# Kernel optimization log

Hardware: AMD Instinct MI355X
Metric: run time of the kernel (lower is better)

The kernel has to match this reference:

```python
import jax, jax.numpy as jnp
import numpy as np

BS, INPUT_LEN, OUTPUT_LEN, H, OUT = 256, 512, 64, 1024, 64


def setup_inputs() -> dict:
    key = jax.random.key(0)
    ks = jax.random.split(key, 13)
    s = 1.0 / np.sqrt(H)
    si = 1.0 / np.sqrt(INPUT_LEN)
    return {
        "is_training": 0,
        "qf_encoded": jax.random.normal(ks[0], (BS, INPUT_LEN, H), jnp.float32),
        "op_encoded": jax.random.normal(ks[1], (BS, OUTPUT_LEN, H), jnp.float32),
        "vocab": jax.random.normal(ks[2], (64, H), jnp.float32),  # unused buffer, kept for fidelity
        "start_token": jax.random.normal(ks[3], (1, H), jnp.float32),
        "w_in": jax.random.uniform(ks[4], (INPUT_LEN,), jnp.float32, -si, si),  # in_proj weight [1, input_len]
        "b_in": jax.random.uniform(ks[5], (1,), jnp.float32, -si, si),
        "w_ih": jax.random.uniform(ks[6], (4 * H, H), jnp.float32, -s, s),
        "w_hh": jax.random.uniform(ks[7], (4 * H, H), jnp.float32, -s, s),
        "b_ih": jax.random.uniform(ks[8], (4 * H,), jnp.float32, -s, s),
        "b_hh": jax.random.uniform(ks[9], (4 * H,), jnp.float32, -s, s),
        "w_out": jax.random.uniform(ks[10], (OUT, H), jnp.float32, -s, s),
        "b_out": jax.random.uniform(ks[11], (OUT,), jnp.float32, -s, s),
    }


def reference(is_training, qf_encoded, op_encoded, vocab, start_token,
              w_in, b_in, w_ih, w_hh, b_ih, b_hh, w_out, b_out):
    # Inference path: dropout is identity, teacher forcing branch never taken
    # (is_training == 0). Attention over the single-step hidden state is
    # computed faithfully even though softmax over a length-1 axis yields 1.
    bs = qf_encoded.shape[0]
    # h0 = in_proj(qf_encoded.transpose(1,2)).squeeze(2): contract over input_len
    h0 = jnp.einsum("bih,i->bh", qf_encoded, w_in) + b_in  # [bs, H]
    c0 = jnp.zeros((bs, H), qf_encoded.dtype)
    x0 = jnp.broadcast_to(start_token, (bs, H))

    def step(carry, _):
        h, c, x = carry
        gates = x @ w_ih.T + b_ih + h @ w_hh.T + b_hh  # [bs, 4H]
        i_g, f_g, g_g, o_g = jnp.split(gates, 4, axis=1)
        c = jax.nn.sigmoid(f_g) * c + jax.nn.sigmoid(i_g) * jnp.tanh(g_g)
        h = jax.nn.sigmoid(o_g) * jnp.tanh(c)
        # attention(x[:,None], h[:,None], h[:,None]): scores [bs,1,1]
        scores = jnp.einsum("bh,bh->b", x, h)[:, None, None]
        w = jax.nn.softmax(scores, axis=2)  # all ones (length-1 softmax)
        x_new = w[:, 0] * h  # [bs,1]*[bs,H] -> [bs,H]
        return (h, c, x_new), h

    (_, _, _), hs = jax.lax.scan(step, (h0, c0, x0), None, length=OUTPUT_LEN)
    output = jnp.transpose(hs, (1, 0, 2))  # [bs, output_len, H]
    probs = output @ w_out.T + b_out  # [bs, output_len, output_size]
    return (probs, output)
```

## Files before the change

### kernel.cpp

```cpp
#include <hip/hip_runtime.h>

#define BS 256
#define IN_LEN 512
#define T_OUT 64
#define H 1024
#define G4 4096

typedef __attribute__((ext_vector_type(8))) short bf16x8;
typedef __attribute__((ext_vector_type(4))) float f32x4;

__device__ __forceinline__ unsigned short f2bf(float x) {
    union { float f; unsigned u; } v; v.f = x;
    unsigned r = v.u + 0x7fffu + ((v.u >> 16) & 1u);
    return (unsigned short)(r >> 16);
}
__device__ __forceinline__ float bf2f(unsigned short b) {
    union { unsigned u; float f; } v; v.u = ((unsigned)b) << 16;
    return v.f;
}
__device__ __forceinline__ float sigf(float x) { return 1.f / (1.f + __expf(-x)); }
__device__ __forceinline__ float tanhfast(float x) { return 1.f - 2.f / (__expf(2.f * x) + 1.f); }

__device__ __forceinline__ void gl_lds16(const void* g, void* l) {
    __builtin_amdgcn_global_load_lds((const __attribute__((address_space(1))) void*)g,
                                     (__attribute__((address_space(3))) void*)l, 16, 0, 0);
}

__global__ __launch_bounds__(256) void k_prep(const float4* __restrict__ w_ih4,
                                              const float4* __restrict__ w_hh4,
                                              const float4* __restrict__ w_out4,
                                              ushort4* __restrict__ Wch, ushort4* __restrict__ Wcl,
                                              ushort4* __restrict__ woh, ushort4* __restrict__ wol) {
    int row = blockIdx.x;
    int c4 = threadIdx.x;
    float4 a = w_ih4[row * 256 + c4];
    float4 b = w_hh4[row * 256 + c4];
    int p = ((row & 1023) << 2) | (row >> 10);
    float sx = a.x + b.x, sy = a.y + b.y, sz = a.z + b.z, sw = a.w + b.w;
    ushort4 hi, lo;
    hi.x = f2bf(sx); lo.x = f2bf(sx - bf2f(hi.x));
    hi.y = f2bf(sy); lo.y = f2bf(sy - bf2f(hi.y));
    hi.z = f2bf(sz); lo.z = f2bf(sz - bf2f(hi.z));
    hi.w = f2bf(sw); lo.w = f2bf(sw - bf2f(hi.w));
    Wch[p * 256 + c4] = hi;
    Wcl[p * 256 + c4] = lo;
    if (row < 64) {
        float4 w = w_out4[row * 256 + c4];
        ushort4 h2, l2;
        h2.x = f2bf(w.x); l2.x = f2bf(w.x - bf2f(h2.x));
        h2.y = f2bf(w.y); l2.y = f2bf(w.y - bf2f(h2.y));
        h2.z = f2bf(w.z); l2.z = f2bf(w.z - bf2f(h2.z));
        h2.w = f2bf(w.w); l2.w = f2bf(w.w - bf2f(h2.w));
        woh[row * 256 + c4] = h2;
        wol[row * 256 + c4] = l2;
    }
}

__global__ __launch_bounds__(256) void k_g0(const float4* __restrict__ st4,
                                            const float4* __restrict__ w_ih4,
                                            const float* __restrict__ b_ih,
                                            const float* __restrict__ b_hh,
                                            float* __restrict__ g0p, float* __restrict__ bcp) {
    int j = (blockIdx.x * 256 + threadIdx.x) >> 6;
    int lane = threadIdx.x & 63;
    float s = 0.f;
#pragma unroll
    for (int q = 0; q < 4; ++q) {
        int idx = q * 64 + lane;
        float4 w4 = w_ih4[(size_t)j * 256 + idx];
        float4 s4 = st4[idx];
        s += w4.x * s4.x + w4.y * s4.y + w4.z * s4.z + w4.w * s4.w;
    }
#pragma unroll
    for (int off = 32; off > 0; off >>= 1) s += __shfl_down(s, off, 64);
    if (lane == 0) {
        int p = ((j & 1023) << 2) | (j >> 10);
        float bb = b_ih[j] + b_hh[j];
        bcp[p] = bb;
        g0p[p] = s + bb;
    }
}

__global__ __launch_bounds__(256) void k_h0(const float4* __restrict__ qf4,
                                            const float* __restrict__ w_in,
                                            const float* __restrict__ b_in,
                                            ushort4* __restrict__ h_hi, ushort4* __restrict__ h_lo,
                                            float4* __restrict__ c4) {
    int idx = blockIdx.x * 256 + threadIdx.x;
    int b = idx >> 8;
    int hq = idx & 255;
    const float4* p = qf4 + (size_t)b * IN_LEN * 256 + hq;
    float4 s = make_float4(0.f, 0.f, 0.f, 0.f);
#pragma unroll 4
    for (int i = 0; i < IN_LEN; ++i) {
        float w = w_in[i];
        float4 q = p[(size_t)i * 256];
        s.x += q.x * w; s.y += q.y * w; s.z += q.z * w; s.w += q.w * w;
    }
    float bi = b_in[0];
    s.x += bi; s.y += bi; s.z += bi; s.w += bi;
    ushort4 hi, lo;
    hi.x = f2bf(s.x); lo.x = f2bf(s.x - bf2f(hi.x));
    hi.y = f2bf(s.y); lo.y = f2bf(s.y - bf2f(hi.y));
    hi.z = f2bf(s.z); lo.z = f2bf(s.z - bf2f(hi.z));
    hi.w = f2bf(s.w); lo.w = f2bf(s.w - bf2f(hi.w));
    h_hi[idx] = hi;
    h_lo[idx] = lo;
    c4[idx] = make_float4(0.f, 0.f, 0.f, 0.f);
}

__global__ __launch_bounds__(256) void k_step(const ushort* __restrict__ Bh,
                                              const ushort* __restrict__ Bl,
                                              const float* __restrict__ Bf,
                                              const float* __restrict__ bias,
                                              const ushort* __restrict__ Ah,
                                              const ushort* __restrict__ Al,
                                              float* __restrict__ c,
                                              ushort* __restrict__ Oh, ushort* __restrict__ Ol,
                                              float* __restrict__ out_h, int t, int useF32) {
    __shared__ __align__(16) ushort sAh[64 * 32], sAl[64 * 32], sBh[64 * 32], sBl[64 * 32];
    __shared__ __align__(16) float sC[64 * 68];

    const int tid = threadIdx.x;
    const int n0 = blockIdx.x * 64;
    const int m0 = blockIdx.y * 64;
    const int w = tid >> 6, l = tid & 63;
    const int wm = w & 1, wn = w >> 1;
    const int lm = l & 15, kg = l >> 4;

    const int srow = tid >> 2;
    const int scol = (tid & 3) * 8;
    const int ldsOff = (tid >> 6) * 512;

    const ushort* gAh = Ah + (m0 + srow) * H + scol;
    const ushort* gAl = Al + (m0 + srow) * H + scol;
    const int prow = n0 + srow;
    const ushort* gBh = Bh + prow * H + scol;
    const ushort* gBl = Bl + prow * H + scol;
    const float* gBf = Bf + ((prow & 3) * H + (prow >> 2)) * H + scol;

    f32x4 acc[2][2];
#pragma unroll
    for (int mi = 0; mi < 2; ++mi)
#pragma unroll
        for (int ni = 0; ni < 2; ++ni) acc[mi][ni] = (f32x4)(0.f);

#pragma unroll 1
    for (int ch = 0; ch < H / 32; ++ch) {
        const int k0 = ch * 32;
        __syncthreads();
        if (useF32) {
            float4 f0 = *(const float4*)(gBf + k0);
            float4 f1 = *(const float4*)(gBf + k0 + 4);
            ushort4 h0_, h1_, l0_, l1_;
            h0_.x = f2bf(f0.x); l0_.x = f2bf(f0.x - bf2f(h0_.x));
            h0_.y = f2bf(f0.y); l0_.y = f2bf(f0.y - bf2f(h0_.y));
            h0_.z = f2bf(f0.z); l0_.z = f2bf(f0.z - bf2f(h0_.z));
            h0_.w = f2bf(f0.w); l0_.w = f2bf(f0.w - bf2f(h0_.w));
            h1_.x = f2bf(f1.x); l1_.x = f2bf(f1.x - bf2f(h1_.x));
            h1_.y = f2bf(f1.y); l1_.y = f2bf(f1.y - bf2f(h1_.y));
            h1_.z = f2bf(f1.z); l1_.z = f2bf(f1.z - bf2f(h1_.z));
            h1_.w = f2bf(f1.w); l1_.w = f2bf(f1.w - bf2f(h1_.w));
            int si = srow * 32 + (tid & 3) * 8;
            *(ushort4*)&sBh[si] = h0_; *(ushort4*)&sBh[si + 4] = h1_;
            *(ushort4*)&sBl[si] = l0_; *(ushort4*)&sBl[si + 4] = l1_;
        } else {
            gl_lds16(gBh + k0, &sBh[ldsOff]);
            gl_lds16(gBl + k0, &sBl[ldsOff]);
        }
        gl_lds16(gAh + k0, &sAh[ldsOff]);
        gl_lds16(gAl + k0, &sAl[ldsOff]);
        __syncthreads();

        bf16x8 ah[2], al[2], bh[2], bl[2];
#pragma unroll
        for (int mi = 0; mi < 2; ++mi) {
            int base = (wm * 32 + mi * 16 + lm) * 32 + kg * 8;
            ah[mi] = *(const bf16x8*)&sAh[base];
            al[mi] = *(const bf16x8*)&sAl[base];
        }
#pragma unroll
        for (int ni = 0; ni < 2; ++ni) {
            int base = (wn * 32 + ni * 16 + lm) * 32 + kg * 8;
            bh[ni] = *(const bf16x8*)&sBh[base];
            bl[ni] = *(const bf16x8*)&sBl[base];
        }
#pragma unroll
        for (int mi = 0; mi < 2; ++mi)
#pragma unroll
            for (int ni = 0; ni < 2; ++ni) {
                acc[mi][ni] = __builtin_amdgcn_mfma_f32_16x16x32_bf16(ah[mi], bh[ni], acc[mi][ni], 0, 0, 0);
                acc[mi][ni] = __builtin_amdgcn_mfma_f32_16x16x32_bf16(ah[mi], bl[ni], acc[mi][ni], 0, 0, 0);
                acc[mi][ni] = __builtin_amdgcn_mfma_f32_16x16x32_bf16(al[mi], bh[ni], acc[mi][ni], 0, 0, 0);
            }
    }

#pragma unroll
    for (int mi = 0; mi < 2; ++mi)
#pragma unroll
        for (int ni = 0; ni < 2; ++ni) {
            int r0 = wm * 32 + mi * 16 + kg * 4;
            int c0_ = wn * 32 + ni * 16 + lm;
#pragma unroll
            for (int r = 0; r < 4; ++r) sC[(r0 + r) * 68 + c0_] = acc[mi][ni][r];
        }
    __syncthreads();

#pragma unroll
    for (int q = 0; q < 4; ++q) {
        int cid = tid + q * 256;
        int bl_ = cid >> 4, hl = cid & 15;
        float4 gv = *(const float4*)&sC[bl_ * 68 + hl * 4];
        float4 bv = *(const float4*)&bias[n0 + hl * 4];
        int b = m0 + bl_;
        int hh = (n0 >> 2) + hl;
        float cold = c[b * H + hh];
        float ig = gv.x + bv.x, fg = gv.y + bv.y, gg = gv.z + bv.z, og = gv.w + bv.w;
        float cn = sigf(fg) * cold + sigf(ig) * tanhfast(gg);
        float hn = sigf(og) * tanhfast(cn);
        c[b * H + hh] = cn;
        unsigned short hb = f2bf(hn);
        Oh[b * H + hh] = hb;
        Ol[b * H + hh] = f2bf(hn - bf2f(hb));
        out_h[(b * T_OUT + t) * H + hh] = hn;
    }
}

__global__ __launch_bounds__(256) void k_probs(const float* __restrict__ hs,
                                               const ushort* __restrict__ Bh,
                                               const ushort* __restrict__ Bl,
                                               const float* __restrict__ b_out,
                                               float* __restrict__ probs) {
    __shared__ __align__(16) ushort sAh[64 * 32], sAl[64 * 32], sBh[64 * 32], sBl[64 * 32];
    const int tid = threadIdx.x;
    const int r0 = blockIdx.x * 64;
    const int w = tid >> 6, l = tid & 63;
    const int wm = w & 1, wn = w >> 1;
    const int lm = l & 15, kg = l >> 4;
    const int srow = tid >> 2;
    const int scol = (tid & 3) * 8;
    const int ldsOff = (tid >> 6) * 512;

    const float* gA = hs + (size_t)(r0 + srow) * H + scol;
    const ushort* gBh = Bh + srow * H + scol;
    const ushort* gBl = Bl + srow * H + scol;

    f32x4 acc[2][2];
#pragma unroll
    for (int mi = 0; mi < 2; ++mi)
#pragma unroll
        for (int ni = 0; ni < 2; ++ni) acc[mi][ni] = (f32x4)(0.f);

#pragma unroll 1
    for (int ch = 0; ch < H / 32; ++ch) {
        const int k0 = ch * 32;
        __syncthreads();
        gl_lds16(gBh + k0, &sBh[ldsOff]);
        gl_lds16(gBl + k0, &sBl[ldsOff]);
        float4 f0 = *(const float4*)(gA + k0);
        float4 f1 = *(const float4*)(gA + k0 + 4);
        ushort4 h0_, h1_, l0_, l1_;
        h0_.x = f2bf(f0.x); l0_.x = f2bf(f0.x - bf2f(h0_.x));
        h0_.y = f2bf(f0.y); l0_.y = f2bf(f0.y - bf2f(h0_.y));
        h0_.z = f2bf(f0.z); l0_.z = f2bf(f0.z - bf2f(h0_.z));
        h0_.w = f2bf(f0.w); l0_.w = f2bf(f0.w - bf2f(h0_.w));
        h1_.x = f2bf(f1.x); l1_.x = f2bf(f1.x - bf2f(h1_.x));
        h1_.y = f2bf(f1.y); l1_.y = f2bf(f1.y - bf2f(h1_.y));
        h1_.z = f2bf(f1.z); l1_.z = f2bf(f1.z - bf2f(h1_.z));
        h1_.w = f2bf(f1.w); l1_.w = f2bf(f1.w - bf2f(h1_.w));
        int si = srow * 32 + (tid & 3) * 8;
        *(ushort4*)&sAh[si] = h0_; *(ushort4*)&sAh[si + 4] = h1_;
        *(ushort4*)&sAl[si] = l0_; *(ushort4*)&sAl[si + 4] = l1_;
        __syncthreads();

        bf16x8 ah[2], al[2], bh[2], bl[2];
#pragma unroll
        for (int mi = 0; mi < 2; ++mi) {
            int base = (wm * 32 + mi * 16 + lm) * 32 + kg * 8;
            ah[mi] = *(const bf16x8*)&sAh[base];
            al[mi] = *(const bf16x8*)&sAl[base];
        }
#pragma unroll
        for (int ni = 0; ni < 2; ++ni) {
            int base = (wn * 32 + ni * 16 + lm) * 32 + kg * 8;
            bh[ni] = *(const bf16x8*)&sBh[base];
            bl[ni] = *(const bf16x8*)&sBl[base];
        }
#pragma unroll
        for (int mi = 0; mi < 2; ++mi)
#pragma unroll
            for (int ni = 0; ni < 2; ++ni) {
                acc[mi][ni] = __builtin_amdgcn_mfma_f32_16x16x32_bf16(ah[mi], bh[ni], acc[mi][ni], 0, 0, 0);
                acc[mi][ni] = __builtin_amdgcn_mfma_f32_16x16x32_bf16(ah[mi], bl[ni], acc[mi][ni], 0, 0, 0);
                acc[mi][ni] = __builtin_amdgcn_mfma_f32_16x16x32_bf16(al[mi], bh[ni], acc[mi][ni], 0, 0, 0);
            }
    }

#pragma unroll
    for (int mi = 0; mi < 2; ++mi)
#pragma unroll
        for (int ni = 0; ni < 2; ++ni) {
            int col = wn * 32 + ni * 16 + lm;
            float bo = b_out[col];
            int rowb = r0 + wm * 32 + mi * 16 + kg * 4;
#pragma unroll
            for (int r = 0; r < 4; ++r)
                probs[(size_t)(rowb + r) * 64 + col] = acc[mi][ni][r] + bo;
        }
}

extern "C" void kernel_launch(void* const* d_in, const int* in_sizes, int n_in,
                              void* d_out, int out_size, void* d_ws, size_t ws_size,
                              hipStream_t stream) {
    const float* qf    = (const float*)d_in[1];
    const float* st    = (const float*)d_in[4];
    const float* w_in  = (const float*)d_in[5];
    const float* b_in  = (const float*)d_in[6];
    const float* w_ih  = (const float*)d_in[7];
    const float* w_hh  = (const float*)d_in[8];
    const float* b_ih  = (const float*)d_in[9];
    const float* b_hh  = (const float*)d_in[10];
    const float* w_out = (const float*)d_in[11];
    const float* b_out = (const float*)d_in[12];

    float* probs = (float*)d_out;
    float* out_h = probs + (size_t)BS * T_OUT * 64;

    char* ws = (char*)d_ws;
    ushort* Wch = (ushort*)ws; ws += (size_t)G4 * H * 2;
    ushort* Wcl = (ushort*)ws; ws += (size_t)G4 * H * 2;
    ushort* woh = (ushort*)ws; ws += (size_t)64 * H * 2;
    ushort* wol = (ushort*)ws; ws += (size_t)64 * H * 2;
    float*  bcp = (float*)ws;  ws += G4 * 4;
    float*  g0p = (float*)ws;  ws += G4 * 4;
    ushort* hAh = (ushort*)ws; ws += (size_t)BS * H * 2;
    ushort* hAl = (ushort*)ws; ws += (size_t)BS * H * 2;
    ushort* hBh = (ushort*)ws; ws += (size_t)BS * H * 2;
    ushort* hBl = (ushort*)ws; ws += (size_t)BS * H * 2;
    float*  cb  = (float*)ws;  ws += (size_t)BS * H * 4;

    k_prep<<<G4, 256, 0, stream>>>((const float4*)w_ih, (const float4*)w_hh, (const float4*)w_out,
                                   (ushort4*)Wch, (ushort4*)Wcl, (ushort4*)woh, (ushort4*)wol);
    k_g0<<<G4 / 4, 256, 0, stream>>>((const float4*)st, (const float4*)w_ih, b_ih, b_hh, g0p, bcp);
    k_h0<<<BS * H / 4 / 256, 256, 0, stream>>>((const float4*)qf, w_in, b_in,
                                               (ushort4*)hAh, (ushort4*)hAl, (float4*)cb);

    for (int t = 0; t < T_OUT; ++t) {
        const ushort* Ah = (t & 1) ? hBh : hAh;
        const ushort* Al = (t & 1) ? hBl : hAl;
        ushort* Oh = (t & 1) ? hAh : hBh;
        ushort* Ol = (t & 1) ? hAl : hBl;
        k_step<<<dim3(64, 4), 256, 0, stream>>>(Wch, Wcl, w_hh,
                                                (t == 0) ? g0p : bcp,
                                                Ah, Al, cb, Oh, Ol, out_h, t, (t == 0) ? 1 : 0);
    }
    k_probs<<<BS * T_OUT / 64, 256, 0, stream>>>(out_h, woh, wol, b_out, probs);
}
```

Baseline: 2.171 ms.

## Fuse LSTM steps and output projection into one persistent cooperative kernel

```diff
diff --git a/kernel.cpp b/kernel.cpp
--- a/kernel.cpp
+++ b/kernel.cpp
@@ -1,10 +1,15 @@
 #include <hip/hip_runtime.h>
+#include <hip/hip_cooperative_groups.h>
+
+namespace cg = cooperative_groups;
 
 #define BS 256
 #define IN_LEN 512
 #define T_OUT 64
 #define H 1024
 #define G4 4096
+#define BK 64
+#define NCH (H / BK)
 
 typedef __attribute__((ext_vector_type(8))) short bf16x8;
 typedef __attribute__((ext_vector_type(4))) float f32x4;
@@ -26,10 +31,14 @@
                                      (__attribute__((address_space(3))) void*)l, 16, 0, 0);
 }
 
+#define FRAG(base, row, ko) \
+    (*(const bf16x8*)((const char*)(base) + ((((row) * 128 + (ko)) ^ ((((row) & 7)) << 4)))))
+
 __global__ __launch_bounds__(256) void k_prep(const float4* __restrict__ w_ih4,
                                               const float4* __restrict__ w_hh4,
                                               const float4* __restrict__ w_out4,
                                               ushort4* __restrict__ Wch, ushort4* __restrict__ Wcl,
+                                              ushort4* __restrict__ Whh, ushort4* __restrict__ Whl,
                                               ushort4* __restrict__ woh, ushort4* __restrict__ wol) {
     int row = blockIdx.x;
     int c4 = threadIdx.x;
@@ -44,15 +53,22 @@
     hi.w = f2bf(sw); lo.w = f2bf(sw - bf2f(hi.w));
     Wch[p * 256 + c4] = hi;
     Wcl[p * 256 + c4] = lo;
+    ushort4 h2, l2;
+    h2.x = f2bf(b.x); l2.x = f2bf(b.x - bf2f(h2.x));
+    h2.y = f2bf(b.y); l2.y = f2bf(b.y - bf2f(h2.y));
+    h2.z = f2bf(b.z); l2.z = f2bf(b.z - bf2f(h2.z));
+    h2.w = f2bf(b.w); l2.w = f2bf(b.w - bf2f(h2.w));
+    Whh[p * 256 + c4] = h2;
+    Whl[p * 256 + c4] = l2;
     if (row < 64) {
         float4 w = w_out4[row * 256 + c4];
-        ushort4 h2, l2;
-        h2.x = f2bf(w.x); l2.x = f2bf(w.x - bf2f(h2.x));
-        h2.y = f2bf(w.y); l2.y = f2bf(w.y - bf2f(h2.y));
-        h2.z = f2bf(w.z); l2.z = f2bf(w.z - bf2f(h2.z));
-        h2.w = f2bf(w.w); l2.w = f2bf(w.w - bf2f(h2.w));
-        woh[row * 256 + c4] = h2;
-        wol[row * 256 + c4] = l2;
+        ushort4 h3, l3;
+        h3.x = f2bf(w.x); l3.x = f2bf(w.x - bf2f(h3.x));
+        h3.y = f2bf(w.y); l3.y = f2bf(w.y - bf2f(h3.y));
+        h3.z = f2bf(w.z); l3.z = f2bf(w.z - bf2f(h3.z));
+        h3.w = f2bf(w.w); l3.w = f2bf(w.w - bf2f(h3.w));
+        woh[row * 256 + c4] = h3;
+        wol[row * 256 + c4] = l3;
     }
 }
 
@@ -81,22 +97,36 @@
     }
 }
 
-__global__ __launch_bounds__(256) void k_h0(const float4* __restrict__ qf4,
-                                            const float* __restrict__ w_in,
-                                            const float* __restrict__ b_in,
-                                            ushort4* __restrict__ h_hi, ushort4* __restrict__ h_lo,
-                                            float4* __restrict__ c4) {
-    int idx = blockIdx.x * 256 + threadIdx.x;
-    int b = idx >> 8;
-    int hq = idx & 255;
-    const float4* p = qf4 + (size_t)b * IN_LEN * 256 + hq;
+__global__ __launch_bounds__(256) void k_h0_part(const float4* __restrict__ qf4,
+                                                 const float* __restrict__ w_in,
+                                                 float4* __restrict__ part) {
+    int b = blockIdx.x >> 2;
+    int kq = blockIdx.x & 3;
+    int hq = threadIdx.x;
+    const float4* p = qf4 + (size_t)b * IN_LEN * 256 + (size_t)kq * 128 * 256 + hq;
+    const float* wv = w_in + kq * 128;
     float4 s = make_float4(0.f, 0.f, 0.f, 0.f);
-#pragma unroll 4
-    for (int i = 0; i < IN_LEN; ++i) {
-        float w = w_in[i];
+#pragma unroll 8
+    for (int i = 0; i < 128; ++i) {
+        float w = wv[i];
         float4 q = p[(size_t)i * 256];
         s.x += q.x * w; s.y += q.y * w; s.z += q.z * w; s.w += q.w * w;
     }
+    part[((size_t)kq * 256 + b) * 256 + hq] = s;
+}
+
+__global__ __launch_bounds__(256) void k_h0_comb(const float4* __restrict__ part,
+                                                 const float* __restrict__ b_in,
+                                                 ushort4* __restrict__ h0h, ushort4* __restrict__ h0l) {
+    int idx = blockIdx.x * 256 + threadIdx.x;
+    float4 s = part[idx];
+    float4 s1 = part[65536 + idx];
+    float4 s2 = part[131072 + idx];
+    float4 s3 = part[196608 + idx];
+    s.x += s1.x + s2.x + s3.x;
+    s.y += s1.y + s2.y + s3.y;
+    s.z += s1.z + s2.z + s3.z;
+    s.w += s1.w + s2.w + s3.w;
     float bi = b_in[0];
     s.x += bi; s.y += bi; s.z += bi; s.w += bi;
     ushort4 hi, lo;
@@ -104,209 +134,189 @@
     hi.y = f2bf(s.y); lo.y = f2bf(s.y - bf2f(hi.y));
     hi.z = f2bf(s.z); lo.z = f2bf(s.z - bf2f(hi.z));
     hi.w = f2bf(s.w); lo.w = f2bf(s.w - bf2f(hi.w));
-    h_hi[idx] = hi;
-    h_lo[idx] = lo;
-    c4[idx] = make_float4(0.f, 0.f, 0.f, 0.f);
-}
-
-__global__ __launch_bounds__(256) void k_step(const ushort* __restrict__ Bh,
-                                              const ushort* __restrict__ Bl,
-                                              const float* __restrict__ Bf,
-                                              const float* __restrict__ bias,
-                                              const ushort* __restrict__ Ah,
-                                              const ushort* __restrict__ Al,
-                                              float* __restrict__ c,
-                                              ushort* __restrict__ Oh, ushort* __restrict__ Ol,
-                                              float* __restrict__ out_h, int t, int useF32) {
-    __shared__ __align__(16) ushort sAh[64 * 32], sAl[64 * 32], sBh[64 * 32], sBl[64 * 32];
+    h0h[idx] = hi;
+    h0l[idx] = lo;
+}
+
+__global__ __launch_bounds__(512, 2) void k_lstm(const ushort* __restrict__ Wch, const ushort* __restrict__ Wcl,
+                                                 const ushort* __restrict__ Whh, const ushort* __restrict__ Whl,
+                                                 const float* __restrict__ g0p, const float* __restrict__ bcp,
+                                                 const ushort* __restrict__ h0h, const ushort* __restrict__ h0l,
+                                                 ushort* __restrict__ hsh, ushort* __restrict__ hsl,
+                                                 const ushort* __restrict__ woh, const ushort* __restrict__ wol,
+                                                 const float* __restrict__ b_out,
+                                                 float* __restrict__ out_h, float* __restrict__ probs) {
+    __shared__ __align__(16) ushort sA[2][2][64 * BK];
+    __shared__ __align__(16) ushort sB[2][2][64 * BK];
     __shared__ __align__(16) float sC[64 * 68];
 
+    cg::grid_group grid = cg::this_grid();
+
     const int tid = threadIdx.x;
-    const int n0 = blockIdx.x * 64;
-    const int m0 = blockIdx.y * 64;
+    const int bid = blockIdx.x;
+    const int n0 = (bid & 63) * 64;
+    const int m0 = (bid >> 6) * 64;
     const int w = tid >> 6, l = tid & 63;
     const int wm = w & 1, wn = w >> 1;
     const int lm = l & 15, kg = l >> 4;
 
-    const int srow = tid >> 2;
-    const int scol = (tid & 3) * 8;
-    const int ldsOff = (tid >> 6) * 512;
-
-    const ushort* gAh = Ah + (m0 + srow) * H + scol;
-    const ushort* gAl = Al + (m0 + srow) * H + scol;
-    const int prow = n0 + srow;
-    const ushort* gBh = Bh + prow * H + scol;
-    const ushort* gBl = Bl + prow * H + scol;
-    const float* gBf = Bf + ((prow & 3) * H + (prow >> 2)) * H + scol;
-
-    f32x4 acc[2][2];
-#pragma unroll
-    for (int mi = 0; mi < 2; ++mi)
-#pragma unroll
-        for (int ni = 0; ni < 2; ++ni) acc[mi][ni] = (f32x4)(0.f);
+    const int srow = (w << 3) + (l >> 3);
+    const int sl8 = ((l & 7) ^ ((l >> 3) & 7)) * 8;
+    const int ldsW = w * 512;
+
+    const size_t obs = (size_t)(n0 + srow) * H + sl8;
+
+    float creg0 = 0.f, creg1 = 0.f;
+
+    const int ra0 = wm * 32 + lm;
+    const int rb = wn * 16 + lm;
 
 #pragma unroll 1
-    for (int ch = 0; ch < H / 32; ++ch) {
-        const int k0 = ch * 32;
+    for (int t = 0; t < T_OUT; ++t) {
+        const ushort* pBh = ((t == 0) ? Whh : Wch) + obs;
+        const ushort* pBl = ((t == 0) ? Whl : Wcl) + obs;
+        const ushort* pAh;
+        const ushort* pAl;
+        if (t == 0) {
+            size_t oa = (size_t)(m0 + srow) * H + sl8;
+            pAh = h0h + oa; pAl = h0l + oa;
+        } else {
+            size_t oa = ((size_t)(m0 + srow) * T_OUT + (t - 1)) * H + sl8;
+            pAh = hsh + oa; pAl = hsl + oa;
+        }
+        const float* bias = (t == 0) ? g0p : bcp;
+
+        f32x4 acc0 = (f32x4)(0.f), acc1 = (f32x4)(0.f);
+
+        gl_lds16(pAh, &sA[0][0][ldsW]);
+        gl_lds16(pAl, &sA[0][1][ldsW]);
+        gl_lds16(pBh, &sB[0][0][ldsW]);
+        gl_lds16(pBh == pBl ? pBl : pBl, &sB[0][1][ldsW]);
         __syncthreads();
-        if (useF32) {
-            float4 f0 = *(const float4*)(gBf + k0);
-            float4 f1 = *(const float4*)(gBf + k0 + 4);
-            ushort4 h0_, h1_, l0_, l1_;
-            h0_.x = f2bf(f0.x); l0_.x = f2bf(f0.x - bf2f(h0_.x));
-            h0_.y = f2bf(f0.y); l0_.y = f2bf(f0.y - bf2f(h0_.y));
-            h0_.z = f2bf(f0.z); l0_.z = f2bf(f0.z - bf2f(h0_.z));
-            h0_.w = f2bf(f0.w); l0_.w = f2bf(f0.w - bf2f(h0_.w));
-            h1_.x = f2bf(f1.x); l1_.x = f2bf(f1.x - bf2f(h1_.x));
-            h1_.y = f2bf(f1.y); l1_.y = f2bf(f1.y - bf2f(h1_.y));
-            h1_.z = f2bf(f1.z); l1_.z = f2bf(f1.z - bf2f(h1_.z));
-            h1_.w = f2bf(f1.w); l1_.w = f2bf(f1.w - bf2f(h1_.w));
-            int si = srow * 32 + (tid & 3) * 8;
-            *(ushort4*)&sBh[si] = h0_; *(ushort4*)&sBh[si + 4] = h1_;
-            *(ushort4*)&sBl[si] = l0_; *(ushort4*)&sBl[si + 4] = l1_;
-        } else {
-            gl_lds16(gBh + k0, &sBh[ldsOff]);
-            gl_lds16(gBl + k0, &sBl[ldsOff]);
-        }
-        gl_lds16(gAh + k0, &sAh[ldsOff]);
-        gl_lds16(gAl + k0, &sAl[ldsOff]);
+
+#pragma unroll 2
+        for (int ch = 0; ch < NCH; ++ch) {
+            const int cur = ch & 1;
+            if (ch + 1 < NCH) {
+                const int k0 = (ch + 1) * BK;
+                gl_lds16(pAh + k0, &sA[cur ^ 1][0][ldsW]);
+                gl_lds16(pAl + k0, &sA[cur ^ 1][1][ldsW]);
+                gl_lds16(pBh + k0, &sB[cur ^ 1][0][ldsW]);
+                gl_lds16(pBl + k0, &sB[cur ^ 1][1][ldsW]);
+            }
+            const ushort* Ah_ = sA[cur][0];
+            const ushort* Al_ = sA[cur][1];
+            const ushort* Bh_ = sB[cur][0];
+            const ushort* Bl_ = sB[cur][1];
+#pragma unroll
+            for (int ks = 0; ks < 2; ++ks) {
+                const int ko = ks * 64 + kg * 16;
+                bf16x8 a0h = FRAG(Ah_, ra0, ko);
+                bf16x8 a0l = FRAG(Al_, ra0, ko);
+                bf16x8 a1h = FRAG(Ah_, ra0 + 16, ko);
+                bf16x8 a1l = FRAG(Al_, ra0 + 16, ko);
+                bf16x8 bh_ = FRAG(Bh_, rb, ko);
+                bf16x8 bl_ = FRAG(Bl_, rb, ko);
+                acc0 = __builtin_amdgcn_mfma_f32_16x16x32_bf16(a0h, bh_, acc0, 0, 0, 0);
+                acc0 = __builtin_amdgcn_mfma_f32_16x16x32_bf16(a0h, bl_, acc0, 0, 0, 0);
+                acc0 = __builtin_amdgcn_mfma_f32_16x16x32_bf16(a0l, bh_, acc0, 0, 0, 0);
+                acc1 = __builtin_amdgcn_mfma_f32_16x16x32_bf16(a1h, bh_, acc1, 0, 0, 0);
+                acc1 = __builtin_amdgcn_mfma_f32_16x16x32_bf16(a1h, bl_, acc1, 0, 0, 0);
+                acc1 = __builtin_amdgcn_mfma_f32_16x16x32_bf16(a1l, bh_, acc1, 0, 0, 0);
+            }
+            __syncthreads();
+        }
+
+        {
+            const int c0 = wn * 16 + lm;
+            const int r0 = wm * 32 + kg * 4;
+#pragma unroll
+            for (int r = 0; r < 4; ++r) sC[(r0 + r) * 68 + c0] = acc0[r];
+#pragma unroll
+            for (int r = 0; r < 4; ++r) sC[(r0 + 16 + r) * 68 + c0] = acc1[r];
+        }
         __syncthreads();
 
-        bf16x8 ah[2], al[2], bh[2], bl[2];
-#pragma unroll
-        for (int mi = 0; mi < 2; ++mi) {
-            int base = (wm * 32 + mi * 16 + lm) * 32 + kg * 8;
-            ah[mi] = *(const bf16x8*)&sAh[base];
-            al[mi] = *(const bf16x8*)&sAl[base];
-        }
-#pragma unroll
-        for (int ni = 0; ni < 2; ++ni) {
-            int base = (wn * 32 + ni * 16 + lm) * 32 + kg * 8;
-            bh[ni] = *(const bf16x8*)&sBh[base];
-            bl[ni] = *(const bf16x8*)&sBl[base];
-        }
-#pragma unroll
-        for (int mi = 0; mi < 2; ++mi)
-#pragma unroll
-            for (int ni = 0; ni < 2; ++ni) {
-                acc[mi][ni] = __builtin_amdgcn_mfma_f32_16x16x32_bf16(ah[mi], bh[ni], acc[mi][ni], 0, 0, 0);
-                acc[mi][ni] = __builtin_amdgcn_mfma_f32_16x16x32_bf16(ah[mi], bl[ni], acc[mi][ni], 0, 0, 0);
-                acc[mi][ni] = __builtin_amdgcn_mfma_f32_16x16x32_bf16(al[mi], bh[ni], acc[mi][ni], 0, 0, 0);
+#pragma unroll
+        for (int q = 0; q < 2; ++q) {
+            int cid = tid + q * 512;
+            int bl_ = cid >> 4, hl = cid & 15;
+            float4 gv = *(const float4*)&sC[bl_ * 68 + hl * 4];
+            float4 bv = *(const float4*)&bias[n0 + hl * 4];
+            float cold = q ? creg1 : creg0;
+            float ig = gv.x + bv.x, fg = gv.y + bv.y, gg = gv.z + bv.z, og = gv.w + bv.w;
+            float cn = sigf(fg) * cold + sigf(ig) * tanhfast(gg);
+            float hn = sigf(og) * tanhfast(cn);
+            if (q) creg1 = cn; else creg0 = cn;
+            int b = m0 + bl_;
+            int hh = (n0 >> 2) + hl;
+            size_t idx = ((size_t)b * T_OUT + t) * H + hh;
+            out_h[idx] = hn;
+            unsigned short hb = f2bf(hn);
+            hsh[idx] = hb;
+            hsl[idx] = f2bf(hn - bf2f(hb));
+        }
+        grid.sync();
+    }
+
+    {
+        size_t oa = ((size_t)(bid * 64 + srow)) * H + sl8;
+        const ushort* pAh = hsh + oa;
+        const ushort* pAl = hsl + oa;
+        const ushort* pBh = woh + (size_t)srow * H + sl8;
+        const ushort* pBl = wol + (size_t)srow * H + sl8;
+
+        f32x4 acc0 = (f32x4)(0.f), acc1 = (f32x4)(0.f);
+
+        gl_lds16(pAh, &sA[0][0][ldsW]);
+        gl_lds16(pAl, &sA[0][1][ldsW]);
+        gl_lds16(pBh, &sB[0][0][ldsW]);
+        gl_lds16(pBl, &sB[0][1][ldsW]);
+        __syncthreads();
+
+#pragma unroll 2
+        for (int ch = 0; ch < NCH; ++ch) {
+            const int cur = ch & 1;
+            if (ch + 1 < NCH) {
+                const int k0 = (ch + 1) * BK;
+                gl_lds16(pAh + k0, &sA[cur ^ 1][0][ldsW]);
+                gl_lds16(pAl + k0, &sA[cur ^ 1][1][ldsW]);
+                gl_lds16(pBh + k0, &sB[cur ^ 1][0][ldsW]);
+                gl_lds16(pBl + k0, &sB[cur ^ 1][1][ldsW]);
             }
-    }
-
-#pragma unroll
-    for (int mi = 0; mi < 2; ++mi)
-#pragma unroll
-        for (int ni = 0; ni < 2; ++ni) {
-            int r0 = wm * 32 + mi * 16 + kg * 4;
-            int c0_ = wn * 32 + ni * 16 + lm;
-#pragma unroll
-            for (int r = 0; r < 4; ++r) sC[(r0 + r) * 68 + c0_] = acc[mi][ni][r];
-        }
-    __syncthreads();
-
-#pragma unroll
-    for (int q = 0; q < 4; ++q) {
-        int cid = tid + q * 256;
-        int bl_ = cid >> 4, hl = cid & 15;
-        float4 gv = *(const float4*)&sC[bl_ * 68 + hl * 4];
-        float4 bv = *(const float4*)&bias[n0 + hl * 4];
-        int b = m0 + bl_;
-        int hh = (n0 >> 2) + hl;
-        float cold = c[b * H + hh];
-        float ig = gv.x + bv.x, fg = gv.y + bv.y, gg = gv.z + bv.z, og = gv.w + bv.w;
-        float cn = sigf(fg) * cold + sigf(ig) * tanhfast(gg);
-        float hn = sigf(og) * tanhfast(cn);
-        c[b * H + hh] = cn;
-        unsigned short hb = f2bf(hn);
-        Oh[b * H + hh] = hb;
-        Ol[b * H + hh] = f2bf(hn - bf2f(hb));
-        out_h[(b * T_OUT + t) * H + hh] = hn;
-    }
-}
-
-__global__ __launch_bounds__(256) void k_probs(const float* __restrict__ hs,
-                                               const ushort* __restrict__ Bh,
-                                               const ushort* __restrict__ Bl,
-                                               const float* __restrict__ b_out,
-                                               float* __restrict__ probs) {
-    __shared__ __align__(16) ushort sAh[64 * 32], sAl[64 * 32], sBh[64 * 32], sBl[64 * 32];
-    const int tid = threadIdx.x;
-    const int r0 = blockIdx.x * 64;
-    const int w = tid >> 6, l = tid & 63;
-    const int wm = w & 1, wn = w >> 1;
-    const int lm = l & 15, kg = l >> 4;
-    const int srow = tid >> 2;
-    const int scol = (tid & 3) * 8;
-    const int ldsOff = (tid >> 6) * 512;
-
-    const float* gA = hs + (size_t)(r0 + srow) * H + scol;
-    const ushort* gBh = Bh + srow * H + scol;
-    const ushort* gBl = Bl + srow * H + scol;
-
-    f32x4 acc[2][2];
-#pragma unroll
-    for (int mi = 0; mi < 2; ++mi)
-#pragma unroll
-        for (int ni = 0; ni < 2; ++ni) acc[mi][ni] = (f32x4)(0.f);
-
-#pragma unroll 1
-    for (int ch = 0; ch < H / 32; ++ch) {
-        const int k0 = ch * 32;
-        __syncthreads();
-        gl_lds16(gBh + k0, &sBh[ldsOff]);
-        gl_lds16(gBl + k0, &sBl[ldsOff]);
-        float4 f0 = *(const float4*)(gA + k0);
-        float4 f1 = *(const float4*)(gA + k0 + 4);
-        ushort4 h0_, h1_, l0_, l1_;
-        h0_.x = f2bf(f0.x); l0_.x = f2bf(f0.x - bf2f(h0_.x));
-        h0_.y = f2bf(f0.y); l0_.y = f2bf(f0.y - bf2f(h0_.y));
-        h0_.z = f2bf(f0.z); l0_.z = f2bf(f0.z - bf2f(h0_.z));
-        h0_.w = f2bf(f0.w); l0_.w = f2bf(f0.w - bf2f(h0_.w));
-        h1_.x = f2bf(f1.x); l1_.x = f2bf(f1.x - bf2f(h1_.x));
-        h1_.y = f2bf(f1.y); l1_.y = f2bf(f1.y - bf2f(h1_.y));
-        h1_.z = f2bf(f1.z); l1_.z = f2bf(f1.z - bf2f(h1_.z));
-        h1_.w = f2bf(f1.w); l1_.w = f2bf(f1.w - bf2f(h1_.w));
-        int si = srow * 32 + (tid & 3) * 8;
-        *(ushort4*)&sAh[si] = h0_; *(ushort4*)&sAh[si + 4] = h1_;
-        *(ushort4*)&sAl[si] = l0_; *(ushort4*)&sAl[si + 4] = l1_;
-        __syncthreads();
-
-        bf16x8 ah[2], al[2], bh[2], bl[2];
-#pragma unroll
-        for (int mi = 0; mi < 2; ++mi) {
-            int base = (wm * 32 + mi * 16 + lm) * 32 + kg * 8;
-            ah[mi] = *(const bf16x8*)&sAh[base];
-            al[mi] = *(const bf16x8*)&sAl[base];
-        }
-#pragma unroll
-        for (int ni = 0; ni < 2; ++ni) {
-            int base = (wn * 32 + ni * 16 + lm) * 32 + kg * 8;
-            bh[ni] = *(const bf16x8*)&sBh[base];
-            bl[ni] = *(const bf16x8*)&sBl[base];
-        }
-#pragma unroll
-        for (int mi = 0; mi < 2; ++mi)
-#pragma unroll
-            for (int ni = 0; ni < 2; ++ni) {
-                acc[mi][ni] = __builtin_amdgcn_mfma_f32_16x16x32_bf16(ah[mi], bh[ni], acc[mi][ni], 0, 0, 0);
-                acc[mi][ni] = __builtin_amdgcn_mfma_f32_16x16x32_bf16(ah[mi], bl[ni], acc[mi][ni], 0, 0, 0);
-                acc[mi][ni] = __builtin_amdgcn_mfma_f32_16x16x32_bf16(al[mi], bh[ni], acc[mi][ni], 0, 0, 0);
+            const ushort* Ah_ = sA[cur][0];
+            const ushort* Al_ = sA[cur][1];
+            const ushort* Bh_ = sB[cur][0];
+            const ushort* Bl_ = sB[cur][1];
+#pragma unroll
+            for (int ks = 0; ks < 2; ++ks) {
+                const int ko = ks * 64 + kg * 16;
+                bf16x8 a0h = FRAG(Ah_, ra0, ko);
+                bf16x8 a0l = FRAG(Al_, ra0, ko);
+                bf16x8 a1h = FRAG(Ah_, ra0 + 16, ko);
+                bf16x8 a1l = FRAG(Al_, ra0 + 16, ko);
+                bf16x8 bh_ = FRAG(Bh_, rb, ko);
+                bf16x8 bl_ = FRAG(Bl_, rb, ko);
+                acc0 = __builtin_amdgcn_mfma_f32_16x16x32_bf16(a0h, bh_, acc0, 0, 0, 0);
+                acc0 = __builtin_amdgcn_mfma_f32_16x16x32_bf16(a0h, bl_, acc0, 0, 0, 0);
+                acc0 = __builtin_amdgcn_mfma_f32_16x16x32_bf16(a0l, bh_, acc0, 0, 0, 0);
+                acc1 = __builtin_amdgcn_mfma_f32_16x16x32_bf16(a1h, bh_, acc1, 0, 0, 0);
+                acc1 = __builtin_amdgcn_mfma_f32_16x16x32_bf16(a1h, bl_, acc1, 0, 0, 0);
+                acc1 = __builtin_amdgcn_mfma_f32_16x16x32_bf16(a1l, bh_, acc1, 0, 0, 0);
             }
-    }
-
-#pragma unroll
-    for (int mi = 0; mi < 2; ++mi)
-#pragma unroll
-        for (int ni = 0; ni < 2; ++ni) {
-            int col = wn * 32 + ni * 16 + lm;
-            float bo = b_out[col];
-            int rowb = r0 + wm * 32 + mi * 16 + kg * 4;
-#pragma unroll
-            for (int r = 0; r < 4; ++r)
-                probs[(size_t)(rowb + r) * 64 + col] = acc[mi][ni][r] + bo;
-        }
+            __syncthreads();
+        }
+
+        const int col = wn * 16 + lm;
+        const float bo = b_out[col];
+        const int rowb = bid * 64 + wm * 32 + kg * 4;
+#pragma unroll
+        for (int r = 0; r < 4; ++r)
+            probs[(size_t)(rowb + r) * 64 + col] = acc0[r] + bo;
+#pragma unroll
+        for (int r = 0; r < 4; ++r)
+            probs[(size_t)(rowb + 16 + r) * 64 + col] = acc1[r] + bo;
+    }
 }
 
 extern "C" void kernel_launch(void* const* d_in, const int* in_sizes, int n_in,
@@ -327,32 +337,30 @@
     float* out_h = probs + (size_t)BS * T_OUT * 64;
 
     char* ws = (char*)d_ws;
-    ushort* Wch = (ushort*)ws; ws += (size_t)G4 * H * 2;
-    ushort* Wcl = (ushort*)ws; ws += (size_t)G4 * H * 2;
-    ushort* woh = (ushort*)ws; ws += (size_t)64 * H * 2;
-    ushort* wol = (ushort*)ws; ws += (size_t)64 * H * 2;
-    float*  bcp = (float*)ws;  ws += G4 * 4;
-    float*  g0p = (float*)ws;  ws += G4 * 4;
-    ushort* hAh = (ushort*)ws; ws += (size_t)BS * H * 2;
-    ushort* hAl = (ushort*)ws; ws += (size_t)BS * H * 2;
-    ushort* hBh = (ushort*)ws; ws += (size_t)BS * H * 2;
-    ushort* hBl = (ushort*)ws; ws += (size_t)BS * H * 2;
-    float*  cb  = (float*)ws;  ws += (size_t)BS * H * 4;
+    ushort* Wch   = (ushort*)ws; ws += (size_t)G4 * H * 2;
+    ushort* Wcl   = (ushort*)ws; ws += (size_t)G4 * H * 2;
+    ushort* Whh_h = (ushort*)ws; ws += (size_t)G4 * H * 2;
+    ushort* Whh_l = (ushort*)ws; ws += (size_t)G4 * H * 2;
+    ushort* woh   = (ushort*)ws; ws += (size_t)64 * H * 2;
+    ushort* wol   = (ushort*)ws; ws += (size_t)64 * H * 2;
+    float*  bcp   = (float*)ws;  ws += G4 * 4;
+    float*  g0p   = (float*)ws;  ws += G4 * 4;
+    ushort* h0h   = (ushort*)ws; ws += (size_t)BS * H * 2;
+    ushort* h0l   = (ushort*)ws; ws += (size_t)BS * H * 2;
+    ushort* hsh   = (ushort*)ws; ws += (size_t)BS * T_OUT * H * 2;
+    ushort* hsl   = (ushort*)ws; ws += (size_t)BS * T_OUT * H * 2;
+    float*  part  = (float*)ws;  ws += (size_t)4 * 256 * 256 * 16;
 
     k_prep<<<G4, 256, 0, stream>>>((const float4*)w_ih, (const float4*)w_hh, (const float4*)w_out,
-                                   (ushort4*)Wch, (ushort4*)Wcl, (ushort4*)woh, (ushort4*)wol);
+                                   (ushort4*)Wch, (ushort4*)Wcl, (ushort4*)Whh_h, (ushort4*)Whh_l,
+                                   (ushort4*)woh, (ushort4*)wol);
     k_g0<<<G4 / 4, 256, 0, stream>>>((const float4*)st, (const float4*)w_ih, b_ih, b_hh, g0p, bcp);
-    k_h0<<<BS * H / 4 / 256, 256, 0, stream>>>((const float4*)qf, w_in, b_in,
-                                               (ushort4*)hAh, (ushort4*)hAl, (float4*)cb);
-
-    for (int t = 0; t < T_OUT; ++t) {
-        const ushort* Ah = (t & 1) ? hBh : hAh;
-        const ushort* Al = (t & 1) ? hBl : hAl;
-        ushort* Oh = (t & 1) ? hAh : hBh;
-        ushort* Ol = (t & 1) ? hAl : hBl;
-        k_step<<<dim3(64, 4), 256, 0, stream>>>(Wch, Wcl, w_hh,
-                                                (t == 0) ? g0p : bcp,
-                                                Ah, Al, cb, Oh, Ol, out_h, t, (t == 0) ? 1 : 0);
-    }
-    k_probs<<<BS * T_OUT / 64, 256, 0, stream>>>(out_h, woh, wol, b_out, probs);
-}
+    k_h0_part<<<BS * 4, 256, 0, stream>>>((const float4*)qf, w_in, (float4*)part);
+    k_h0_comb<<<BS, 256, 0, stream>>>((const float4*)part, b_in, (ushort4*)h0h, (ushort4*)h0l);
+
+    void* args[] = {(void*)&Wch, (void*)&Wcl, (void*)&Whh_h, (void*)&Whh_l,
+                    (void*)&g0p, (void*)&bcp, (void*)&h0h, (void*)&h0l,
+                    (void*)&hsh, (void*)&hsl, (void*)&woh, (void*)&wol,
+                    (void*)&b_out, (void*)&out_h, (void*)&probs};
+    hipLaunchCooperativeKernel(k_lstm, dim3(256), dim3(512), args, 0, stream);
+}
```

Result: slower. 3.735 ms (+72.0%).
